# Kernel optimization log

Hardware: AMD Instinct MI355X
Metric: run time of the kernel (lower is better)

The kernel has to match this reference:

```python
import jax, jax.numpy as jnp
import numpy as np

B, C, N = 8, 512, 2048
D = C // 8  # query/key dim


def setup_inputs() -> dict:
    key = jax.random.key(0)
    ks = jax.random.split(key, 6)
    x = jax.random.normal(ks[0], (B, C, N), dtype=jnp.float32)
    mask = jax.random.uniform(ks[1], (B, N), dtype=jnp.float32)
    Wq = jax.random.normal(ks[2], (D, C), dtype=jnp.float32) * (1.0 / np.sqrt(C))
    Wk = jax.random.normal(ks[3], (D, C), dtype=jnp.float32) * (1.0 / np.sqrt(C))
    Wv = jax.random.normal(ks[4], (C, C), dtype=jnp.float32) * (1.0 / np.sqrt(C))
    gamma = jax.random.normal(ks[5], (1,), dtype=jnp.float32)
    return {"x": x, "mask": mask, "Wq": Wq, "Wk": Wk, "Wv": Wv, "gamma": gamma}


def reference(x, mask, Wq, Wk, Wv, gamma):
    # 1x1 Conv1d (no bias) == channel matmul: (out,in) @ (B,in,N) -> (B,out,N)
    f = jnp.einsum('dc,bcn->bdn', Wq, x)   # query  (B, D, N)
    g = jnp.einsum('dc,bcn->bdn', Wk, x)   # key    (B, D, N)
    h = jnp.einsum('oc,bcn->bon', Wv, x)   # value  (B, C, N)
    # scores = f^T @ g : (B, N, N); act == identity ('none')
    scores = jnp.einsum('bdn,bdm->bnm', f, g)
    # column softmax: softmax over dim=1 (rows, i.e. first N axis)
    beta = jax.nn.softmax(scores, axis=1)  # (B, N, N)
    # post-softmax mask + renormalization over the same axis
    beta = beta * mask[:, :, None]
    beta = beta / (jnp.sum(beta, axis=1, keepdims=True) + 1e-12)
    # o = gamma * (h @ beta) + x
    o = gamma * jnp.einsum('bcn,bnm->bcm', h, beta) + x
    return o
```

## Files before the change

kernel.cpp:

```cpp
#include <hip/hip_runtime.h>
#include <hip/hip_bf16.h>

#define BB 8
#define CC 512
#define NN 2048
#define DD 64

typedef __attribute__((ext_vector_type(8))) _Float16 f16x8;
typedef __attribute__((ext_vector_type(4))) _Float16 f16x4;
typedef __attribute__((ext_vector_type(4))) float f32x4;

#define WS_WF 0u
#define WS_FT 1048576u
#define WS_GT 3145728u
#define WS_H  5242880u
#define WS_M  22020096u
#define WS_S  22151168u

#define HS0 0
#define FS0 65536
#define BT0 81920
#define LDS2B 114688

static __device__ __forceinline__ void gload_lds16(const void* g, void* l) {
    __builtin_amdgcn_global_load_lds(
        (const __attribute__((address_space(1))) void*)g,
        (__attribute__((address_space(3))) void*)l, 16, 0, 0);
}

static __device__ __forceinline__ void hard_barrier() {
    __builtin_amdgcn_sched_barrier(0);
    __builtin_amdgcn_s_barrier();
    __builtin_amdgcn_sched_barrier(0);
}

__global__ __launch_bounds__(256) void wconv_kernel(
    const float* __restrict__ Wq, const float* __restrict__ Wk,
    const float* __restrict__ Wv, _Float16* __restrict__ Wf)
{
    int e = (blockIdx.x * 256 + threadIdx.x) * 8;
    const float* src;
    if (e < 32768) src = Wq + e;
    else if (e < 65536) src = Wk + (e - 32768);
    else src = Wv + (e - 65536);
    float4 v0 = *reinterpret_cast<const float4*>(src);
    float4 v1 = *reinterpret_cast<const float4*>(src + 4);
    f16x8 o = {(_Float16)v0.x, (_Float16)v0.y, (_Float16)v0.z, (_Float16)v0.w,
               (_Float16)v1.x, (_Float16)v1.y, (_Float16)v1.z, (_Float16)v1.w};
    *reinterpret_cast<f16x8*>(Wf + e) = o;
}

__global__ __launch_bounds__(512, 2) void proj_kernel(
    const float* __restrict__ x, const _Float16* __restrict__ Wf,
    const float* __restrict__ mask,
    _Float16* __restrict__ fT, _Float16* __restrict__ gT, _Float16* __restrict__ h)
{
    const int nb = blockIdx.x, b = blockIdx.y;
    const int n0 = nb * 64;
    const int t = threadIdx.x, w = t >> 6, l = t & 63, lo = l & 15, hi = l >> 4;

    __shared__ _Float16 xs[64][512];

    const float* xb = x + (size_t)b * CC * NN + n0;
    {
        const int cq = t >> 4, nq = t & 15;
        #pragma unroll 4
        for (int p = 0; p < 16; p++) {
            int c = 32 * p + cq;
            float4 v = *reinterpret_cast<const float4*>(xb + (size_t)c * NN + 4 * nq);
            int cc = c >> 3, cb = c & 7;
            float vv[4] = {v.x, v.y, v.z, v.w};
            #pragma unroll
            for (int j = 0; j < 4; j++) {
                int n = 4 * nq + j;
                xs[n][(((cc ^ (n & 7)) << 3) | cb)] = (_Float16)vv[j];
            }
        }
    }
    __syncthreads();

    f32x4 acc[5][4];
    #pragma unroll
    for (int i = 0; i < 5; i++)
        #pragma unroll
        for (int j = 0; j < 4; j++) acc[i][j] = (f32x4){0.f, 0.f, 0.f, 0.f};

    #pragma unroll 4
    for (int ks = 0; ks < 16; ks++) {
        f16x8 bfr[4];
        #pragma unroll
        for (int nf = 0; nf < 4; nf++)
            bfr[nf] = *reinterpret_cast<const f16x8*>(
                &xs[16 * nf + lo][((4 * ks + hi) ^ (lo & 7)) << 3]);
        #pragma unroll
        for (int rf = 0; rf < 5; rf++) {
            f16x8 af = *reinterpret_cast<const f16x8*>(
                Wf + (size_t)(16 * (w + 8 * rf) + lo) * CC + 32 * ks + 8 * hi);
            #pragma unroll
            for (int nf = 0; nf < 4; nf++)
                acc[rf][nf] = __builtin_amdgcn_mfma_f32_16x16x32_f16(af, bfr[nf], acc[rf][nf], 0, 0, 0);
        }
    }

    float mask4[4];
    #pragma unroll
    for (int nf = 0; nf < 4; nf++) mask4[nf] = mask[(size_t)b * NN + n0 + 16 * nf + lo];

    #pragma unroll
    for (int rf = 0; rf < 5; rf++) {
        int Rb = 16 * (w + 8 * rf);
        #pragma unroll
        for (int nf = 0; nf < 4; nf++) {
            int n = n0 + 16 * nf + lo;
            if (Rb < 64) {
                f16x4 v = {(_Float16)acc[rf][nf][0], (_Float16)acc[rf][nf][1],
                           (_Float16)acc[rf][nf][2], (_Float16)acc[rf][nf][3]};
                *reinterpret_cast<f16x4*>(&fT[((size_t)b * NN + n) * DD + Rb + 4 * hi]) = v;
            } else if (Rb < 128) {
                f16x4 v = {(_Float16)acc[rf][nf][0], (_Float16)acc[rf][nf][1],
                           (_Float16)acc[rf][nf][2], (_Float16)acc[rf][nf][3]};
                *reinterpret_cast<f16x4*>(&gT[((size_t)b * NN + n) * DD + (Rb - 64) + 4 * hi]) = v;
            } else {
                int cr = Rb - 128 + 4 * hi;
                #pragma unroll
                for (int j = 0; j < 4; j++)
                    h[((size_t)b * CC + cr + j) * NN + n] = (_Float16)(acc[rf][nf][j] * mask4[nf]);
            }
        }
    }
}

__global__ __launch_bounds__(512, 2) void stats_kernel(
    const _Float16* __restrict__ fT, const _Float16* __restrict__ gT,
    const float* __restrict__ mask, float* __restrict__ Mp, float* __restrict__ Sp)
{
    const int bid = blockIdx.x;
    const int b = bid & 7, mb = (bid >> 3) & 31, ns = bid >> 8;
    const int m0 = mb * 64;
    const int t = threadIdx.x, w = t >> 6, l = t & 63, lo = l & 15, hi = l >> 4;

    __shared__ float masks_l[1024];
    __shared__ float sm[8][64], ss[8][64];

    *reinterpret_cast<float2*>(&masks_l[2 * t]) =
        *reinterpret_cast<const float2*>(&mask[(size_t)b * NN + ns * 1024 + 2 * t]);
    __syncthreads();

    const _Float16* gTb = gT + (size_t)b * NN * DD;
    const _Float16* fTb = fT + ((size_t)b * NN + ns * 1024) * DD;

    f16x8 bq[4][2];
    #pragma unroll
    for (int mf = 0; mf < 4; mf++)
        #pragma unroll
        for (int kk = 0; kk < 2; kk++)
            bq[mf][kk] = *reinterpret_cast<const f16x8*>(
                gTb + (size_t)(m0 + 16 * mf + lo) * DD + 32 * kk + 8 * hi);

    float m_run[4] = {-1e30f, -1e30f, -1e30f, -1e30f};
    float s_run[4] = {0.f, 0.f, 0.f, 0.f};

    #pragma unroll
    for (int tl = 0; tl < 2; tl++) {
        const int nl = (w + 8 * tl) * 64;
        f16x8 afr[4][2];
        #pragma unroll
        for (int rf = 0; rf < 4; rf++)
            #pragma unroll
            for (int kk = 0; kk < 2; kk++)
                afr[rf][kk] = *reinterpret_cast<const f16x8*>(
                    fTb + (size_t)(nl + 16 * rf + lo) * DD + 32 * kk + 8 * hi);
        #pragma unroll
        for (int mf = 0; mf < 4; mf++) {
            f32x4 s4[4];
            #pragma unroll
            for (int rf = 0; rf < 4; rf++) {
                f32x4 a4 = (f32x4){0.f, 0.f, 0.f, 0.f};
                a4 = __builtin_amdgcn_mfma_f32_16x16x32_f16(afr[rf][0], bq[mf][0], a4, 0, 0, 0);
                a4 = __builtin_amdgcn_mfma_f32_16x16x32_f16(afr[rf][1], bq[mf][1], a4, 0, 0, 0);
                s4[rf] = a4;
            }
            float mx = -1e30f;
            #pragma unroll
            for (int rf = 0; rf < 4; rf++)
                #pragma unroll
                for (int j = 0; j < 4; j++) mx = fmaxf(mx, s4[rf][j]);
            float nm = fmaxf(m_run[mf], mx);
            float sum = 0.f;
            #pragma unroll
            for (int rf = 0; rf < 4; rf++)
                #pragma unroll
                for (int j = 0; j < 4; j++)
                    sum += masks_l[nl + 16 * rf + 4 * hi + j] * __expf(s4[rf][j] - nm);
            s_run[mf] = s_run[mf] * __expf(m_run[mf] - nm) + sum;
            m_run[mf] = nm;
        }
    }
    #pragma unroll
    for (int mf = 0; mf < 4; mf++) {
        #pragma unroll
        for (int d = 16; d <= 32; d <<= 1) {
            float om = __shfl_xor(m_run[mf], d);
            float os = __shfl_xor(s_run[mf], d);
            float nm = fmaxf(m_run[mf], om);
            s_run[mf] = s_run[mf] * __expf(m_run[mf] - nm) + os * __expf(om - nm);
            m_run[mf] = nm;
        }
    }
    if (l < 16) {
        #pragma unroll
        for (int mf = 0; mf < 4; mf++) { sm[w][16 * mf + l] = m_run[mf]; ss[w][16 * mf + l] = s_run[mf]; }
    }
    __syncthreads();
    if (t < 64) {
        float M = -1e30f;
        #pragma unroll
        for (int w8 = 0; w8 < 8; w8++) M = fmaxf(M, sm[w8][t]);
        float S = 0.f;
        #pragma unroll
        for (int w8 = 0; w8 < 8; w8++) S += ss[w8][t] * __expf(sm[w8][t] - M);
        Mp[(size_t)(ns * 8 + b) * NN + m0 + t] = M;
        Sp[(size_t)(ns * 8 + b) * NN + m0 + t] = S;
    }
}

__global__ __launch_bounds__(512, 1) void attn2_kernel(
    const _Float16* __restrict__ fT, const _Float16* __restrict__ gT,
    const _Float16* __restrict__ h, const float* __restrict__ x,
    const float* __restrict__ Mp, const float* __restrict__ Sp,
    const float* __restrict__ gamma, float* __restrict__ out)
{
    extern __shared__ __align__(16) char smem[];
    const int bid = blockIdx.x;
    const int b = bid & 7, mb2 = (bid >> 3) & 15, cs2 = bid >> 7;
    const int m0 = mb2 * 128, cbase = cs2 * 256;
    const int t = threadIdx.x, w = t >> 6, l = t & 63, lo = l & 15, hi = l >> 4;
    const int r3 = l >> 3, c3 = l & 7, sch = c3 ^ r3;
    const int sn = 32 * (w & 1), smg = 32 * (w >> 1);
    const int cg = w & 3, mg = w >> 2;

    const _Float16* hb = h + (size_t)b * CC * NN;
    const _Float16* fTb = fT + (size_t)b * NN * DD;

    f16x8 bq[2][2]; float Mr[2], iSr[2];
    #pragma unroll
    for (int mf = 0; mf < 2; mf++) {
        int m = m0 + smg + 16 * mf + lo;
        #pragma unroll
        for (int kk = 0; kk < 2; kk++)
            bq[mf][kk] = *reinterpret_cast<const f16x8*>(
                gT + ((size_t)b * NN + m) * DD + 32 * kk + 8 * hi);
        float M0 = Mp[(size_t)b * NN + m],       S0 = Sp[(size_t)b * NN + m];
        float M1 = Mp[(size_t)(8 + b) * NN + m], S1 = Sp[(size_t)(8 + b) * NN + m];
        float M = fmaxf(M0, M1);
        float S = S0 * __expf(M0 - M) + S1 * __expf(M1 - M);
        Mr[mf] = M; iSr[mf] = 1.0f / (S + 1e-20f);
    }

    f32x4 o[4][4];
    #pragma unroll
    for (int ci = 0; ci < 4; ci++)
        #pragma unroll
        for (int mi = 0; mi < 4; mi++) o[ci][mi] = (f32x4){0.f, 0.f, 0.f, 0.f};

    #define STAGE(ti, bs) do {                                                         \
        const int _n0 = (ti) * 64;                                                     \
        char* _hd = smem + (bs) * 32768 + (32 * w) * 128;                              \
        const _Float16* _hs = hb + (size_t)(cbase + 32 * w + r3) * NN + _n0 + sch * 8; \
        _Pragma("unroll")                                                              \
        for (int _q = 0; _q < 4; _q++)                                                 \
            gload_lds16((const void*)(_hs + (size_t)(8 * _q) * NN), (void*)(_hd + _q * 1024)); \
        char* _fd = smem + FS0 + (bs) * 8192 + (8 * w) * 128;                          \
        const _Float16* _fs = fTb + (size_t)(_n0 + 8 * w + r3) * DD + sch * 8;         \
        gload_lds16((const void*)_fs, (void*)_fd);                                     \
    } while (0)

    STAGE(0, 0);

    #pragma unroll 1
    for (int i = 0; i < 32; i++) {
        const int cur = i & 1;
        asm volatile("s_waitcnt vmcnt(0)" ::: "memory");
        hard_barrier();
        if (i < 31) STAGE(i + 1, cur ^ 1);

        char* fsb = smem + FS0 + cur * 8192;
        char* btb = smem + BT0 + cur * 16384;
        f32x4 s4[2][2];
        #pragma unroll
        for (int rf = 0; rf < 2; rf++)
            #pragma unroll
            for (int mf = 0; mf < 2; mf++) s4[rf][mf] = (f32x4){0.f, 0.f, 0.f, 0.f};
        #pragma unroll
        for (int rf = 0; rf < 2; rf++) {
            int nrow = sn + 16 * rf + lo;
            #pragma unroll
            for (int kk = 0; kk < 2; kk++) {
                f16x8 af = *reinterpret_cast<const f16x8*>(
                    fsb + nrow * 128 + (((4 * kk + hi) ^ (lo & 7)) << 4));
                #pragma unroll
                for (int mf = 0; mf < 2; mf++)
                    s4[rf][mf] = __builtin_amdgcn_mfma_f32_16x16x32_f16(af, bq[mf][kk], s4[rf][mf], 0, 0, 0);
            }
        }
        #pragma unroll
        for (int rf = 0; rf < 2; rf++)
            #pragma unroll
            for (int mf = 0; mf < 2; mf++) {
                f16x4 ev;
                #pragma unroll
                for (int j = 0; j < 4; j++)
                    ev[j] = (_Float16)(__expf(s4[rf][mf][j] - Mr[mf]) * iSr[mf]);
                int ml = smg + 16 * mf + lo;
                int nl = sn + 16 * rf + 4 * hi;
                int chunk = (nl >> 3) ^ (lo & 7);
                *reinterpret_cast<f16x4*>(btb + ml * 128 + chunk * 16 + (nl & 7) * 2) = ev;
            }
        asm volatile("s_waitcnt lgkmcnt(0)" ::: "memory");
        hard_barrier();

        char* hsb = smem + cur * 32768;
        #pragma unroll
        for (int kk = 0; kk < 2; kk++) {
            f16x8 bb[4];
            #pragma unroll
            for (int mi = 0; mi < 4; mi++) {
                int ml = 64 * mg + 16 * mi + lo;
                bb[mi] = *reinterpret_cast<const f16x8*>(
                    btb + ml * 128 + (((4 * kk + hi) ^ (lo & 7)) << 4));
            }
            #pragma unroll
            for (int ci = 0; ci < 4; ci++) {
                int crow = 64 * cg + 16 * ci + lo;
                f16x8 ah = *reinterpret_cast<const f16x8*>(
                    hsb + crow * 128 + (((4 * kk + hi) ^ (lo & 7)) << 4));
                #pragma unroll
                for (int mi = 0; mi < 4; mi++)
                    o[ci][mi] = __builtin_amdgcn_mfma_f32_16x16x32_f16(ah, bb[mi], o[ci][mi], 0, 0, 0);
            }
        }
    }
    #undef STAGE

    __syncthreads();

    float* ob = reinterpret_cast<float*>(smem + w * 9216);
    const float gm = gamma[0];
    const float* xb = x + (size_t)b * CC * NN;
    float* outb = out + (size_t)b * CC * NN;

    #pragma unroll
    for (int half = 0; half < 2; half++) {
        #pragma unroll
        for (int ci = 0; ci < 4; ci++)
            #pragma unroll
            for (int mh = 0; mh < 2; mh++) {
                int mi = 2 * half + mh;
                #pragma unroll
                for (int j = 0; j < 4; j++) {
                    int row = 16 * ci + 4 * hi + j;
                    int ml = 16 * mh + lo;
                    ob[row * 36 + (((ml >> 2) ^ (row & 7)) << 2) + (ml & 3)] = o[ci][mi][j];
                }
            }
        asm volatile("s_waitcnt lgkmcnt(0)" ::: "memory");
        #pragma unroll
        for (int rr = 0; rr < 8; rr++) {
            int row = 8 * rr + r3;
            f32x4 v = *reinterpret_cast<const f32x4*>(ob + row * 36 + ((c3 ^ (row & 7)) << 2));
            size_t idx = (size_t)(cbase + 64 * cg + row) * NN + m0 + 64 * mg + 32 * half + 4 * c3;
            float4 xv = *reinterpret_cast<const float4*>(xb + idx);
            float4 res;
            res.x = gm * v[0] + xv.x; res.y = gm * v[1] + xv.y;
            res.z = gm * v[2] + xv.z; res.w = gm * v[3] + xv.w;
            *reinterpret_cast<float4*>(outb + idx) = res;
        }
        asm volatile("s_waitcnt lgkmcnt(0)" ::: "memory");
    }
}

extern "C" void kernel_launch(void* const* d_in, const int* in_sizes, int n_in,
                              void* d_out, int out_size, void* d_ws, size_t ws_size,
                              hipStream_t stream) {
    (void)in_sizes; (void)n_in; (void)out_size; (void)ws_size;
    const float* x     = (const float*)d_in[0];
    const float* mask  = (const float*)d_in[1];
    const float* Wq    = (const float*)d_in[2];
    const float* Wk    = (const float*)d_in[3];
    const float* Wv    = (const float*)d_in[4];
    const float* gamma = (const float*)d_in[5];
    float* out = (float*)d_out;

    char* ws = (char*)d_ws;
    _Float16* Wf = (_Float16*)(ws + WS_WF);
    _Float16* fT = (_Float16*)(ws + WS_FT);
    _Float16* gT = (_Float16*)(ws + WS_GT);
    _Float16* h  = (_Float16*)(ws + WS_H);
    float* Mp = (float*)(ws + WS_M);
    float* Sp = (float*)(ws + WS_S);

    wconv_kernel<<<160, 256, 0, stream>>>(Wq, Wk, Wv, Wf);
    proj_kernel<<<dim3(32, 8), 512, 0, stream>>>(x, Wf, mask, fT, gT, h);
    stats_kernel<<<512, 512, 0, stream>>>(fT, gT, mask, Mp, Sp);
    hipFuncSetAttribute((const void*)attn2_kernel,
                        hipFuncAttributeMaxDynamicSharedMemorySize, LDS2B);
    attn2_kernel<<<256, 512, LDS2B, stream>>>(fT, gT, h, x, Mp, Sp, gamma, out);
}
```

Baseline: 188.1 us.

## Triple-buffer attention staging, split stats wider, vectorize proj transpose, direct epilogue

The attention kernel now keeps three h/fT stage buffers with a prefetch distance of two and waits on a partial vmcnt, so global loads overlap more compute. Each warp now computes a 16x64 score tile instead of 32x32, and the LDS-staged output epilogue is replaced by direct scalar global stores. The stats kernel is split into four N-slices over 1024 blocks with no running-max loop, and the attention kernel combines the four partial max/sum pairs. The proj kernel now loads four channels at a time and writes f16x4 vectors into the swizzled LDS transpose. Risks are higher LDS use, which may lower occupancy, and uncoalesced scalar output stores.

```diff
diff --git a/kernel.cpp b/kernel.cpp
--- a/kernel.cpp
+++ b/kernel.cpp
@@ -15,12 +15,12 @@
 #define WS_GT 3145728u
 #define WS_H  5242880u
 #define WS_M  22020096u
-#define WS_S  22151168u
-
-#define HS0 0
-#define FS0 65536
-#define BT0 81920
-#define LDS2B 114688
+#define WS_S  22282240u
+
+#define HSOFF(bf) ((bf) * 32768)
+#define FSOFF(bf) (98304 + (bf) * 8192)
+#define BTOFF(bf) (122880 + (bf) * 16384)
+#define LDS2B 155648
 
 static __device__ __forceinline__ void gload_lds16(const void* g, void* l) {
     __builtin_amdgcn_global_load_lds(
@@ -59,22 +59,28 @@
     const int n0 = nb * 64;
     const int t = threadIdx.x, w = t >> 6, l = t & 63, lo = l & 15, hi = l >> 4;
 
-    __shared__ _Float16 xs[64][512];
+    __shared__ _Float16 xs[64 * 512];
 
     const float* xb = x + (size_t)b * CC * NN + n0;
     {
-        const int cq = t >> 4, nq = t & 15;
-        #pragma unroll 4
-        for (int p = 0; p < 16; p++) {
-            int c = 32 * p + cq;
-            float4 v = *reinterpret_cast<const float4*>(xb + (size_t)c * NN + 4 * nq);
-            int cc = c >> 3, cb = c & 7;
-            float vv[4] = {v.x, v.y, v.z, v.w};
-            #pragma unroll
-            for (int j = 0; j < 4; j++) {
-                int n = 4 * nq + j;
-                xs[n][(((cc ^ (n & 7)) << 3) | cb)] = (_Float16)vv[j];
-            }
+        const int nq = t & 15, cqi = t >> 4;
+        #pragma unroll
+        for (int p = 0; p < 4; p++) {
+            int c0 = 128 * p + 4 * cqi;
+            float4 v0 = *reinterpret_cast<const float4*>(xb + (size_t)(c0 + 0) * NN + 4 * nq);
+            float4 v1 = *reinterpret_cast<const float4*>(xb + (size_t)(c0 + 1) * NN + 4 * nq);
+            float4 v2 = *reinterpret_cast<const float4*>(xb + (size_t)(c0 + 2) * NN + 4 * nq);
+            float4 v3 = *reinterpret_cast<const float4*>(xb + (size_t)(c0 + 3) * NN + 4 * nq);
+            int cc = c0 >> 3, cb = c0 & 7;
+            f16x4 t0 = {(_Float16)v0.x, (_Float16)v1.x, (_Float16)v2.x, (_Float16)v3.x};
+            f16x4 t1 = {(_Float16)v0.y, (_Float16)v1.y, (_Float16)v2.y, (_Float16)v3.y};
+            f16x4 t2 = {(_Float16)v0.z, (_Float16)v1.z, (_Float16)v2.z, (_Float16)v3.z};
+            f16x4 t3 = {(_Float16)v0.w, (_Float16)v1.w, (_Float16)v2.w, (_Float16)v3.w};
+            int n = 4 * nq;
+            *reinterpret_cast<f16x4*>(&xs[(n + 0) * 512 + (((cc ^ ((n + 0) & 7)) << 3) | cb)]) = t0;
+            *reinterpret_cast<f16x4*>(&xs[(n + 1) * 512 + (((cc ^ ((n + 1) & 7)) << 3) | cb)]) = t1;
+            *reinterpret_cast<f16x4*>(&xs[(n + 2) * 512 + (((cc ^ ((n + 2) & 7)) << 3) | cb)]) = t2;
+            *reinterpret_cast<f16x4*>(&xs[(n + 3) * 512 + (((cc ^ ((n + 3) & 7)) << 3) | cb)]) = t3;
         }
     }
     __syncthreads();
@@ -89,9 +95,11 @@
     for (int ks = 0; ks < 16; ks++) {
         f16x8 bfr[4];
         #pragma unroll
-        for (int nf = 0; nf < 4; nf++)
+        for (int nf = 0; nf < 4; nf++) {
+            int row = 16 * nf + lo;
             bfr[nf] = *reinterpret_cast<const f16x8*>(
-                &xs[16 * nf + lo][((4 * ks + hi) ^ (lo & 7)) << 3]);
+                &xs[row * 512 + (((4 * ks + hi) ^ (row & 7)) << 3)]);
+        }
         #pragma unroll
         for (int rf = 0; rf < 5; rf++) {
             f16x8 af = *reinterpret_cast<const f16x8*>(
@@ -130,7 +138,7 @@
     }
 }
 
-__global__ __launch_bounds__(512, 2) void stats_kernel(
+__global__ __launch_bounds__(512) void stats_kernel(
     const _Float16* __restrict__ fT, const _Float16* __restrict__ gT,
     const float* __restrict__ mask, float* __restrict__ Mp, float* __restrict__ Sp)
 {
@@ -139,15 +147,14 @@
     const int m0 = mb * 64;
     const int t = threadIdx.x, w = t >> 6, l = t & 63, lo = l & 15, hi = l >> 4;
 
-    __shared__ float masks_l[1024];
+    __shared__ float masks_l[512];
     __shared__ float sm[8][64], ss[8][64];
 
-    *reinterpret_cast<float2*>(&masks_l[2 * t]) =
-        *reinterpret_cast<const float2*>(&mask[(size_t)b * NN + ns * 1024 + 2 * t]);
+    masks_l[t] = mask[(size_t)b * NN + ns * 512 + t];
     __syncthreads();
 
     const _Float16* gTb = gT + (size_t)b * NN * DD;
-    const _Float16* fTb = fT + ((size_t)b * NN + ns * 1024) * DD;
+    const _Float16* fTb = fT + ((size_t)b * NN + ns * 512 + 64 * w) * DD;
 
     f16x8 bq[4][2];
     #pragma unroll
@@ -157,44 +164,37 @@
             bq[mf][kk] = *reinterpret_cast<const f16x8*>(
                 gTb + (size_t)(m0 + 16 * mf + lo) * DD + 32 * kk + 8 * hi);
 
-    float m_run[4] = {-1e30f, -1e30f, -1e30f, -1e30f};
-    float s_run[4] = {0.f, 0.f, 0.f, 0.f};
-
-    #pragma unroll
-    for (int tl = 0; tl < 2; tl++) {
-        const int nl = (w + 8 * tl) * 64;
-        f16x8 afr[4][2];
+    f16x8 afr[4][2];
+    #pragma unroll
+    for (int rf = 0; rf < 4; rf++)
+        #pragma unroll
+        for (int kk = 0; kk < 2; kk++)
+            afr[rf][kk] = *reinterpret_cast<const f16x8*>(
+                fTb + (size_t)(16 * rf + lo) * DD + 32 * kk + 8 * hi);
+
+    float m_run[4], s_run[4];
+    #pragma unroll
+    for (int mf = 0; mf < 4; mf++) {
+        f32x4 s4[4];
+        #pragma unroll
+        for (int rf = 0; rf < 4; rf++) {
+            f32x4 a4 = (f32x4){0.f, 0.f, 0.f, 0.f};
+            a4 = __builtin_amdgcn_mfma_f32_16x16x32_f16(afr[rf][0], bq[mf][0], a4, 0, 0, 0);
+            a4 = __builtin_amdgcn_mfma_f32_16x16x32_f16(afr[rf][1], bq[mf][1], a4, 0, 0, 0);
+            s4[rf] = a4;
+        }
+        float mx = -1e30f;
         #pragma unroll
         for (int rf = 0; rf < 4; rf++)
             #pragma unroll
-            for (int kk = 0; kk < 2; kk++)
-                afr[rf][kk] = *reinterpret_cast<const f16x8*>(
-                    fTb + (size_t)(nl + 16 * rf + lo) * DD + 32 * kk + 8 * hi);
-        #pragma unroll
-        for (int mf = 0; mf < 4; mf++) {
-            f32x4 s4[4];
-            #pragma unroll
-            for (int rf = 0; rf < 4; rf++) {
-                f32x4 a4 = (f32x4){0.f, 0.f, 0.f, 0.f};
-                a4 = __builtin_amdgcn_mfma_f32_16x16x32_f16(afr[rf][0], bq[mf][0], a4, 0, 0, 0);
-                a4 = __builtin_amdgcn_mfma_f32_16x16x32_f16(afr[rf][1], bq[mf][1], a4, 0, 0, 0);
-                s4[rf] = a4;
-            }
-            float mx = -1e30f;
-            #pragma unroll
-            for (int rf = 0; rf < 4; rf++)
-                #pragma unroll
-                for (int j = 0; j < 4; j++) mx = fmaxf(mx, s4[rf][j]);
-            float nm = fmaxf(m_run[mf], mx);
-            float sum = 0.f;
-            #pragma unroll
-            for (int rf = 0; rf < 4; rf++)
-                #pragma unroll
-                for (int j = 0; j < 4; j++)
-                    sum += masks_l[nl + 16 * rf + 4 * hi + j] * __expf(s4[rf][j] - nm);
-            s_run[mf] = s_run[mf] * __expf(m_run[mf] - nm) + sum;
-            m_run[mf] = nm;
-        }
+            for (int j = 0; j < 4; j++) mx = fmaxf(mx, s4[rf][j]);
+        float sum = 0.f;
+        #pragma unroll
+        for (int rf = 0; rf < 4; rf++)
+            #pragma unroll
+            for (int j = 0; j < 4; j++)
+                sum += masks_l[64 * w + 16 * rf + 4 * hi + j] * __expf(s4[rf][j] - mx);
+        m_run[mf] = mx; s_run[mf] = sum;
     }
     #pragma unroll
     for (int mf = 0; mf < 4; mf++) {
@@ -232,28 +232,33 @@
 {
     extern __shared__ __align__(16) char smem[];
     const int bid = blockIdx.x;
-    const int b = bid & 7, mb2 = (bid >> 3) & 15, cs2 = bid >> 7;
-    const int m0 = mb2 * 128, cbase = cs2 * 256;
+    const int b = bid & 7, mb = (bid >> 3) & 15, cs = bid >> 7;
+    const int m0 = mb * 128, cbase = cs * 256;
     const int t = threadIdx.x, w = t >> 6, l = t & 63, lo = l & 15, hi = l >> 4;
     const int r3 = l >> 3, c3 = l & 7, sch = c3 ^ r3;
-    const int sn = 32 * (w & 1), smg = 32 * (w >> 1);
+    const int sn = 16 * (w & 3), smg = 64 * (w >> 2);
     const int cg = w & 3, mg = w >> 2;
 
     const _Float16* hb = h + (size_t)b * CC * NN;
     const _Float16* fTb = fT + (size_t)b * NN * DD;
 
-    f16x8 bq[2][2]; float Mr[2], iSr[2];
-    #pragma unroll
-    for (int mf = 0; mf < 2; mf++) {
+    f16x8 bq[4][2]; float Mr[4], iSr[4];
+    #pragma unroll
+    for (int mf = 0; mf < 4; mf++) {
         int m = m0 + smg + 16 * mf + lo;
         #pragma unroll
         for (int kk = 0; kk < 2; kk++)
             bq[mf][kk] = *reinterpret_cast<const f16x8*>(
                 gT + ((size_t)b * NN + m) * DD + 32 * kk + 8 * hi);
-        float M0 = Mp[(size_t)b * NN + m],       S0 = Sp[(size_t)b * NN + m];
-        float M1 = Mp[(size_t)(8 + b) * NN + m], S1 = Sp[(size_t)(8 + b) * NN + m];
-        float M = fmaxf(M0, M1);
-        float S = S0 * __expf(M0 - M) + S1 * __expf(M1 - M);
+        float Ms[4], Ss[4];
+        #pragma unroll
+        for (int ns = 0; ns < 4; ns++) {
+            Ms[ns] = Mp[(size_t)(ns * 8 + b) * NN + m];
+            Ss[ns] = Sp[(size_t)(ns * 8 + b) * NN + m];
+        }
+        float M = fmaxf(fmaxf(Ms[0], Ms[1]), fmaxf(Ms[2], Ms[3]));
+        float S = Ss[0] * __expf(Ms[0] - M) + Ss[1] * __expf(Ms[1] - M)
+                + Ss[2] * __expf(Ms[2] - M) + Ss[3] * __expf(Ms[3] - M);
         Mr[mf] = M; iSr[mf] = 1.0f / (S + 1e-20f);
     }
 
@@ -263,63 +268,51 @@
         #pragma unroll
         for (int mi = 0; mi < 4; mi++) o[ci][mi] = (f32x4){0.f, 0.f, 0.f, 0.f};
 
-    #define STAGE(ti, bs) do {                                                         \
-        const int _n0 = (ti) * 64;                                                     \
-        char* _hd = smem + (bs) * 32768 + (32 * w) * 128;                              \
-        const _Float16* _hs = hb + (size_t)(cbase + 32 * w + r3) * NN + _n0 + sch * 8; \
-        _Pragma("unroll")                                                              \
-        for (int _q = 0; _q < 4; _q++)                                                 \
+    #define STAGE(ti, bs) do {                                                          \
+        char* _fd = smem + FSOFF(bs) + (8 * w) * 128;                                   \
+        const _Float16* _fs = fTb + (size_t)((ti) * 64 + 8 * w + r3) * DD + sch * 8;    \
+        gload_lds16((const void*)_fs, (void*)_fd);                                      \
+        char* _hd = smem + HSOFF(bs) + (32 * w) * 128;                                  \
+        const _Float16* _hs = hb + (size_t)(cbase + 32 * w + r3) * NN + (ti) * 64 + sch * 8; \
+        _Pragma("unroll")                                                               \
+        for (int _q = 0; _q < 4; _q++)                                                  \
             gload_lds16((const void*)(_hs + (size_t)(8 * _q) * NN), (void*)(_hd + _q * 1024)); \
-        char* _fd = smem + FS0 + (bs) * 8192 + (8 * w) * 128;                          \
-        const _Float16* _fs = fTb + (size_t)(_n0 + 8 * w + r3) * DD + sch * 8;         \
-        gload_lds16((const void*)_fs, (void*)_fd);                                     \
     } while (0)
 
     STAGE(0, 0);
+    STAGE(1, 1);
 
     #pragma unroll 1
     for (int i = 0; i < 32; i++) {
-        const int cur = i & 1;
-        asm volatile("s_waitcnt vmcnt(0)" ::: "memory");
+        if (i == 31) asm volatile("s_waitcnt vmcnt(0)" ::: "memory");
+        else         asm volatile("s_waitcnt vmcnt(5)" ::: "memory");
         hard_barrier();
-        if (i < 31) STAGE(i + 1, cur ^ 1);
-
-        char* fsb = smem + FS0 + cur * 8192;
-        char* btb = smem + BT0 + cur * 16384;
-        f32x4 s4[2][2];
-        #pragma unroll
-        for (int rf = 0; rf < 2; rf++)
-            #pragma unroll
-            for (int mf = 0; mf < 2; mf++) s4[rf][mf] = (f32x4){0.f, 0.f, 0.f, 0.f};
-        #pragma unroll
-        for (int rf = 0; rf < 2; rf++) {
-            int nrow = sn + 16 * rf + lo;
-            #pragma unroll
-            for (int kk = 0; kk < 2; kk++) {
-                f16x8 af = *reinterpret_cast<const f16x8*>(
-                    fsb + nrow * 128 + (((4 * kk + hi) ^ (lo & 7)) << 4));
-                #pragma unroll
-                for (int mf = 0; mf < 2; mf++)
-                    s4[rf][mf] = __builtin_amdgcn_mfma_f32_16x16x32_f16(af, bq[mf][kk], s4[rf][mf], 0, 0, 0);
-            }
-        }
-        #pragma unroll
-        for (int rf = 0; rf < 2; rf++)
-            #pragma unroll
-            for (int mf = 0; mf < 2; mf++) {
+        if (i <= 29) STAGE(i + 2, (i + 2) % 3);
+
+        char* fsb = smem + FSOFF(i % 3);
+        char* btb = smem + BTOFF(i & 1);
+        {
+            int arow = sn + lo;
+            f16x8 af0 = *reinterpret_cast<const f16x8*>(fsb + arow * 128 + ((hi ^ (lo & 7)) << 4));
+            f16x8 af1 = *reinterpret_cast<const f16x8*>(fsb + arow * 128 + (((4 + hi) ^ (lo & 7)) << 4));
+            #pragma unroll
+            for (int mf = 0; mf < 4; mf++) {
+                f32x4 a4 = (f32x4){0.f, 0.f, 0.f, 0.f};
+                a4 = __builtin_amdgcn_mfma_f32_16x16x32_f16(af0, bq[mf][0], a4, 0, 0, 0);
+                a4 = __builtin_amdgcn_mfma_f32_16x16x32_f16(af1, bq[mf][1], a4, 0, 0, 0);
                 f16x4 ev;
                 #pragma unroll
                 for (int j = 0; j < 4; j++)
-                    ev[j] = (_Float16)(__expf(s4[rf][mf][j] - Mr[mf]) * iSr[mf]);
+                    ev[j] = (_Float16)(__expf(a4[j] - Mr[mf]) * iSr[mf]);
                 int ml = smg + 16 * mf + lo;
-                int nl = sn + 16 * rf + 4 * hi;
-                int chunk = (nl >> 3) ^ (lo & 7);
-                *reinterpret_cast<f16x4*>(btb + ml * 128 + chunk * 16 + (nl & 7) * 2) = ev;
-            }
+                int chunk = (2 * (w & 3) + (hi >> 1)) ^ (lo & 7);
+                *reinterpret_cast<f16x4*>(btb + ml * 128 + chunk * 16 + (hi & 1) * 8) = ev;
+            }
+        }
         asm volatile("s_waitcnt lgkmcnt(0)" ::: "memory");
         hard_barrier();
 
-        char* hsb = smem + cur * 32768;
+        char* hsb = smem + HSOFF(i % 3);
         #pragma unroll
         for (int kk = 0; kk < 2; kk++) {
             f16x8 bb[4];
@@ -342,41 +335,20 @@
     }
     #undef STAGE
 
-    __syncthreads();
-
-    float* ob = reinterpret_cast<float*>(smem + w * 9216);
     const float gm = gamma[0];
     const float* xb = x + (size_t)b * CC * NN;
     float* outb = out + (size_t)b * CC * NN;
-
-    #pragma unroll
-    for (int half = 0; half < 2; half++) {
-        #pragma unroll
-        for (int ci = 0; ci < 4; ci++)
-            #pragma unroll
-            for (int mh = 0; mh < 2; mh++) {
-                int mi = 2 * half + mh;
-                #pragma unroll
-                for (int j = 0; j < 4; j++) {
-                    int row = 16 * ci + 4 * hi + j;
-                    int ml = 16 * mh + lo;
-                    ob[row * 36 + (((ml >> 2) ^ (row & 7)) << 2) + (ml & 3)] = o[ci][mi][j];
-                }
-            }
-        asm volatile("s_waitcnt lgkmcnt(0)" ::: "memory");
-        #pragma unroll
-        for (int rr = 0; rr < 8; rr++) {
-            int row = 8 * rr + r3;
-            f32x4 v = *reinterpret_cast<const f32x4*>(ob + row * 36 + ((c3 ^ (row & 7)) << 2));
-            size_t idx = (size_t)(cbase + 64 * cg + row) * NN + m0 + 64 * mg + 32 * half + 4 * c3;
-            float4 xv = *reinterpret_cast<const float4*>(xb + idx);
-            float4 res;
-            res.x = gm * v[0] + xv.x; res.y = gm * v[1] + xv.y;
-            res.z = gm * v[2] + xv.z; res.w = gm * v[3] + xv.w;
-            *reinterpret_cast<float4*>(outb + idx) = res;
-        }
-        asm volatile("s_waitcnt lgkmcnt(0)" ::: "memory");
-    }
+    #pragma unroll
+    for (int ci = 0; ci < 4; ci++)
+        #pragma unroll
+        for (int mi = 0; mi < 4; mi++)
+            #pragma unroll
+            for (int j = 0; j < 4; j++) {
+                int c = cbase + 64 * cg + 16 * ci + 4 * hi + j;
+                int m = m0 + 64 * mg + 16 * mi + lo;
+                size_t idx = (size_t)c * NN + m;
+                outb[idx] = gm * o[ci][mi][j] + xb[idx];
+            }
 }
 
 extern "C" void kernel_launch(void* const* d_in, const int* in_sizes, int n_in,
@@ -401,7 +373,7 @@
 
     wconv_kernel<<<160, 256, 0, stream>>>(Wq, Wk, Wv, Wf);
     proj_kernel<<<dim3(32, 8), 512, 0, stream>>>(x, Wf, mask, fT, gT, h);
-    stats_kernel<<<512, 512, 0, stream>>>(fT, gT, mask, Mp, Sp);
+    stats_kernel<<<1024, 512, 0, stream>>>(fT, gT, mask, Mp, Sp);
     hipFuncSetAttribute((const void*)attn2_kernel,
                         hipFuncAttributeMaxDynamicSharedMemorySize, LDS2B);
     attn2_kernel<<<256, 512, LDS2B, stream>>>(fT, gT, h, x, Mp, Sp, gamma, out);
```

After: 193.8 us. 1.03x slower.
